# Optimization experiments

Hardware: AMD Instinct MI355X
Metric: run time of the kernel (lower is better)

Reference implementation:

```python
import jax, jax.numpy as jnp
import numpy as np

ALPHA = 0.5
ITER_NUM = 3
SV_NUM = 2
EPS_NORM = 1e-12  # torch F.normalize eps
EPS_DIV = 1e-5
B, D, N = 256, 256, 1024


def _l2norm(t, axis):
    # matches torch F.normalize: t / max(||t||, eps)
    n = jnp.sqrt(jnp.sum(t * t, axis=axis, keepdims=True))
    return t / jnp.maximum(n, EPS_NORM)


def setup_inputs() -> dict:
    key = jax.random.key(0)
    k1, k2 = jax.random.split(key)
    x = jax.random.normal(k1, (B, D, N), dtype=jnp.float32)
    weight = jax.random.normal(k2, (D,), dtype=jnp.float32)
    return {"x": x, "weight": weight}


def reference(x, weight):
    b, d, n = x.shape
    xt = jnp.swapaxes(x, 1, 2)  # (b, N, d) -- matches x.transpose(1, 2)
    us, ss, vs = [], [], []
    s = None
    for _ in range(SV_NUM):  # deflation loop over top singular components
        v = jnp.broadcast_to(weight[None, :, None], (b, d, 1))
        for _ in range(ITER_NUM):  # power iteration
            u = _l2norm(xt @ v, axis=1)                      # (b, N, 1)
            v = _l2norm(jnp.swapaxes(xt, 1, 2) @ u, axis=1)  # (b, d, 1)
        s = jnp.swapaxes(u, 1, 2) @ xt @ v                   # (b, 1, 1) spectral value
        us.append(u)
        ss.append(s.reshape(b, 1))
        vs.append(v)
        # rank-1 deflation: x <- x - u s v^T
        xt = xt - s * (u @ jnp.swapaxes(v, 1, 2))
    U = jnp.concatenate(us, axis=-1)   # (b, N, top)
    V = jnp.concatenate(vs, axis=-1)   # (b, d, top)
    S = jnp.concatenate(ss, axis=-1)   # (b, top)
    # y = U diag(S^alpha) V^T, plus the power-normalized residual
    y = jnp.einsum('bnk,bk,bdk->bnd', U, S ** ALPHA, V)      # (b, N, d)
    y = y + xt / (s ** (1.0 - ALPHA) + EPS_DIV)              # norm_remain branch
    y = jnp.swapaxes(y, 1, 2)                                # (b, d, N)
    return y.reshape(b, -1)                                  # vec == 'full'
```

## Files before the change

### kernel.cpp

```cpp
#include <hip/hip_runtime.h>

#define NB 256
#define ND 256
#define NN 1024

typedef _Float16 f16_t;
typedef _Float16 f16x8 __attribute__((ext_vector_type(8)));
typedef float    f32x4 __attribute__((ext_vector_type(4)));
typedef float    f32x16 __attribute__((ext_vector_type(16)));

__global__ __launch_bounds__(512, 2) void k1_gram(const float* __restrict__ x,
                                                  f16_t* __restrict__ g)
{
    __shared__ __align__(16) f16_t sbuf[2][256 * 64];

    const int t = threadIdx.x;
    const int b = blockIdx.x;
    const float* xb = x + (size_t)b * ND * NN;

    const int c8    = t & 7;
    const int rbase = t >> 3;

    f32x4 pf[8];

    auto issue = [&](int kc) {
        const float* base = xb + (size_t)kc * 64 + c8 * 8;
        #pragma unroll
        for (int kk = 0; kk < 4; ++kk) {
            const float* p = base + (size_t)(rbase + 64 * kk) * NN;
            pf[2 * kk]     = *(const f32x4*)p;
            pf[2 * kk + 1] = *(const f32x4*)(p + 4);
        }
    };
    auto commit = [&](int buf) {
        #pragma unroll
        for (int kk = 0; kk < 4; ++kk) {
            const int row = rbase + 64 * kk;
            f16x8 h;
            #pragma unroll
            for (int j = 0; j < 4; ++j) {
                h[j]     = (f16_t)pf[2 * kk][j];
                h[4 + j] = (f16_t)pf[2 * kk + 1][j];
            }
            *(f16x8*)&sbuf[buf][row * 64 + ((c8 ^ (row & 7)) << 3)] = h;
        }
    };

    const int w     = t >> 6;
    const int lane  = t & 63;
    const int mbase = (w & 3) * 64;
    const int nbase = (w >> 2) * 128;
    const int fr    = lane & 31;
    const int half  = lane >> 5;

    f32x16 acc[2][4] = {};

    issue(0);
    commit(0);

    for (int kc = 0; kc < 16; ++kc) {
        __syncthreads();
        if (kc < 15) issue(kc + 1);
        const f16_t* sb = sbuf[kc & 1];
        #pragma unroll
        for (int ks = 0; ks < 4; ++ks) {
            const int ch = ks * 2 + half;
            f16x8 bf[4];
            #pragma unroll
            for (int nb = 0; nb < 4; ++nb) {
                const int row = nbase + nb * 32 + fr;
                bf[nb] = *(const f16x8*)&sb[row * 64 + ((ch ^ (row & 7)) << 3)];
            }
            #pragma unroll
            for (int mb = 0; mb < 2; ++mb) {
                const int row = mbase + mb * 32 + fr;
                const f16x8 af = *(const f16x8*)&sb[row * 64 + ((ch ^ (row & 7)) << 3)];
                #pragma unroll
                for (int nb = 0; nb < 4; ++nb)
                    acc[mb][nb] = __builtin_amdgcn_mfma_f32_32x32x16_f16(
                        af, bf[nb], acc[mb][nb], 0, 0, 0);
            }
        }
        if (kc < 15) commit((kc + 1) & 1);
    }

    f16_t* gb = g + (size_t)b * ND * ND;
    #pragma unroll
    for (int mb = 0; mb < 2; ++mb)
        #pragma unroll
        for (int nb = 0; nb < 4; ++nb) {
            const int gcol = nbase + nb * 32 + fr;
            #pragma unroll
            for (int r = 0; r < 16; ++r) {
                const int grow = mbase + mb * 32 + (r & 3) + 8 * (r >> 2) + 4 * half;
                gb[grow * ND + gcol] = (f16_t)acc[mb][nb][r];
            }
        }
}

__global__ __launch_bounds__(512, 1) void k2_power(const f16_t* __restrict__ g,
                                                   const float* __restrict__ wvec,
                                                   float* __restrict__ vecs,
                                                   float* __restrict__ pars)
{
    __shared__ float sv[ND];
    __shared__ float sv1[ND];
    __shared__ float sred[8];

    const int t = threadIdx.x;
    const int b = blockIdx.x;
    const int r = t >> 1;
    const int h = t & 1;

    const f16_t* gr = g + (size_t)b * ND * ND + (size_t)r * ND + h * 128;
    f16x8 g8[16];
    #pragma unroll
    for (int i = 0; i < 16; ++i) g8[i] = *(const f16x8*)(gr + i * 8);

    auto reduce = [&](float val) -> float {
        #pragma unroll
        for (int off = 32; off > 0; off >>= 1) val += __shfl_xor(val, off, 64);
        __syncthreads();
        if ((t & 63) == 0) sred[t >> 6] = val;
        __syncthreads();
        float s = 0.f;
        #pragma unroll
        for (int i = 0; i < 8; ++i) s += sred[i];
        return s;
    };

    auto rowdot = [&](void) -> float {
        float acc = 0.f;
        const float* svh = sv + h * 128;
        #pragma unroll
        for (int i = 0; i < 16; ++i) {
            const f32x4 va = *(const f32x4*)&svh[i * 8];
            const f32x4 vb = *(const f32x4*)&svh[i * 8 + 4];
            #pragma unroll
            for (int j = 0; j < 4; ++j) {
                acc += (float)g8[i][j]     * va[j];
                acc += (float)g8[i][4 + j] * vb[j];
            }
        }
        acc += __shfl_xor(acc, 1, 64);
        return acc;
    };

    if (h == 0) sv[r] = wvec[r];
    __syncthreads();

    float s1 = 0.f, n1 = 1.f;
    for (int it = 0; it < 3; ++it) {
        const float p  = rowdot();
        const float pp = reduce(0.5f * p * p);
        const float nrm = fmaxf(sqrtf(pp), 1e-12f);
        if (it == 2) {
            const float pv = reduce(0.5f * p * sv[r]);
            n1 = sqrtf(pv);
            s1 = sqrtf(pp) / n1;
            if (h == 0) {
                vecs[((size_t)b * 4 + 0) * ND + r] = sv[r];
                vecs[((size_t)b * 4 + 2) * ND + r] = p / nrm;
            }
            sv1[r] = p / nrm;
        }
        if (h == 0) sv[r] = p / nrm;
        __syncthreads();
    }

    if (h == 0) sv[r] = wvec[r];
    __syncthreads();

    float s2 = 0.f, n2 = 1.f, d1b = 0.f;
    const float s1sq = s1 * s1;
    for (int it = 0; it < 3; ++it) {
        const float d1 = reduce(0.5f * sv1[r] * sv[r]);
        const float p  = rowdot() - s1sq * d1 * sv1[r];
        const float pp = reduce(0.5f * p * p);
        const float nrm = fmaxf(sqrtf(pp), 1e-12f);
        if (it == 2) {
            const float pv = reduce(0.5f * p * sv[r]);
            n2  = sqrtf(pv);
            s2  = sqrtf(pp) / n2;
            d1b = d1;
            if (h == 0) {
                vecs[((size_t)b * 4 + 1) * ND + r] = sv[r];
                vecs[((size_t)b * 4 + 3) * ND + r] = p / nrm;
            }
        }
        if (h == 0) sv[r] = p / nrm;
        __syncthreads();
    }

    if (t == 0) {
        const float rr = 1.f / (sqrtf(s2) + 1e-5f);
        float* pb = pars + b * 8;
        pb[0] = 1.f / n1;
        pb[1] = 1.f / n2;
        pb[2] = s1 * d1b / n2;
        pb[3] = rr;
        pb[4] = sqrtf(s1) - s1 * rr;
        pb[5] = sqrtf(s2) - s2 * rr;
        pb[6] = s1;
        pb[7] = s2;
    }
}

__global__ __launch_bounds__(256, 2) void k3_out(const float* __restrict__ x,
                                                 const float* __restrict__ vecs,
                                                 const float* __restrict__ pars,
                                                 float* __restrict__ y)
{
    __shared__ float sva[ND], svb[ND], sv1[ND], sv2[ND];
    __shared__ float spr1[16][64], spr2[16][64];
    __shared__ float sg1[64], sg2[64];
    __shared__ float spar[8];

    const int t  = threadIdx.x;
    const int b  = blockIdx.x >> 4;
    const int n0 = (blockIdx.x & 15) * 64;

    {
        const float* vb = vecs + (size_t)b * 4 * ND;
        sva[t] = vb[t];
        svb[t] = vb[ND + t];
        sv1[t] = vb[2 * ND + t];
        sv2[t] = vb[3 * ND + t];
        if (t < 8) spar[t] = pars[b * 8 + t];
    }

    const int c4 = t & 15;
    const int rg = t >> 4;
    const float* xb = x + (size_t)b * ND * NN + n0 + c4 * 4;

    f32x4 xr[16];
    #pragma unroll
    for (int k = 0; k < 16; ++k)
        xr[k] = *(const f32x4*)(xb + (size_t)(rg + 16 * k) * NN);

    __syncthreads();

    f32x4 a1 = {0.f, 0.f, 0.f, 0.f}, a2 = {0.f, 0.f, 0.f, 0.f};
    #pragma unroll
    for (int k = 0; k < 16; ++k) {
        const int row = rg + 16 * k;
        a1 += xr[k] * sva[row];
        a2 += xr[k] * svb[row];
    }
    *(f32x4*)&spr1[rg][c4 * 4] = a1;
    *(f32x4*)&spr2[rg][c4 * 4] = a2;
    __syncthreads();

    if (t < 64) {
        float u1 = 0.f, u2 = 0.f;
        #pragma unroll
        for (int g2 = 0; g2 < 16; ++g2) { u1 += spr1[g2][t]; u2 += spr2[g2][t]; }
        const float uu1 = u1 * spar[0];
        const float uu2 = u2 * spar[1] - spar[2] * uu1;
        sg1[t] = spar[4] * uu1;
        sg2[t] = spar[5] * uu2;
    }
    __syncthreads();

    const float rr = spar[3];
    const f32x4 g1 = *(const f32x4*)&sg1[c4 * 4];
    const f32x4 g2 = *(const f32x4*)&sg2[c4 * 4];
    float* yb = y + (size_t)b * ND * NN + n0 + c4 * 4;
    #pragma unroll
    for (int k = 0; k < 16; ++k) {
        const int row = rg + 16 * k;
        const f32x4 o = xr[k] * rr + g1 * sv1[row] + g2 * sv2[row];
        *(f32x4*)(yb + (size_t)row * NN) = o;
    }
}

extern "C" void kernel_launch(void* const* d_in, const int* in_sizes, int n_in,
                              void* d_out, int out_size, void* d_ws, size_t ws_size,
                              hipStream_t stream)
{
    const float* x = (const float*)d_in[0];
    const float* w = (const float*)d_in[1];
    float* out = (float*)d_out;

    f16_t* G = (f16_t*)d_out;

    float* vecs = (float*)d_ws;
    float* pars = vecs + (size_t)NB * 4 * ND;

    k1_gram<<<dim3(NB), dim3(512), 0, stream>>>(x, G);
    k2_power<<<dim3(NB), dim3(512), 0, stream>>>(G, w, vecs, pars);
    k3_out<<<dim3(NB * 16), dim3(256), 0, stream>>>(x, vecs, pars, out);
}
```

Measured before the change: 545.2 us.

## Fuse Gram, power iteration and output kernels into one per-batch kernel

Merges the three kernels into a single per-batch block. The Gram matrix stays in shared memory with a swizzled layout instead of going through global memory, and the power-iteration vectors and parameters stay in LDS. The output phase loops over 16 column tiles and prefetches the next x tile into registers. This removes the global round trips for G, vecs and pars and two kernel launches. In exchange there are only 256 blocks, LDS use is large (128KB plus extras), which may limit occupancy to one block per CU, and the output phase loses the parallelism of the 4096-block grid.

Result: no change. 549.8 us (+0.9%).

```diff
diff --git a/kernel.cpp b/kernel.cpp
--- a/kernel.cpp
+++ b/kernel.cpp
@@ -9,113 +9,122 @@
 typedef float    f32x4 __attribute__((ext_vector_type(4)));
 typedef float    f32x16 __attribute__((ext_vector_type(16)));
 
-__global__ __launch_bounds__(512, 2) void k1_gram(const float* __restrict__ x,
-                                                  f16_t* __restrict__ g)
+__global__ __launch_bounds__(512, 2) void k_fused(const float* __restrict__ x,
+                                                  const float* __restrict__ wvec,
+                                                  float* __restrict__ y)
 {
-    __shared__ __align__(16) f16_t sbuf[2][256 * 64];
+    __shared__ __align__(16) unsigned char smem[131072];
+    __shared__ float sv[ND], sv1v[ND], sva[ND], svb[ND];
+    __shared__ float sred[8], spar[8], sg1[64], sg2[64];
 
     const int t = threadIdx.x;
     const int b = blockIdx.x;
     const float* xb = x + (size_t)b * ND * NN;
 
-    const int c8    = t & 7;
-    const int rbase = t >> 3;
-
-    f32x4 pf[8];
-
-    auto issue = [&](int kc) {
-        const float* base = xb + (size_t)kc * 64 + c8 * 8;
-        #pragma unroll
-        for (int kk = 0; kk < 4; ++kk) {
-            const float* p = base + (size_t)(rbase + 64 * kk) * NN;
-            pf[2 * kk]     = *(const f32x4*)p;
-            pf[2 * kk + 1] = *(const f32x4*)(p + 4);
-        }
-    };
-    auto commit = [&](int buf) {
-        #pragma unroll
-        for (int kk = 0; kk < 4; ++kk) {
-            const int row = rbase + 64 * kk;
-            f16x8 h;
-            #pragma unroll
-            for (int j = 0; j < 4; ++j) {
-                h[j]     = (f16_t)pf[2 * kk][j];
-                h[4 + j] = (f16_t)pf[2 * kk + 1][j];
-            }
-            *(f16x8*)&sbuf[buf][row * 64 + ((c8 ^ (row & 7)) << 3)] = h;
-        }
-    };
-
-    const int w     = t >> 6;
-    const int lane  = t & 63;
-    const int mbase = (w & 3) * 64;
-    const int nbase = (w >> 2) * 128;
-    const int fr    = lane & 31;
-    const int half  = lane >> 5;
-
-    f32x16 acc[2][4] = {};
-
-    issue(0);
-    commit(0);
-
-    for (int kc = 0; kc < 16; ++kc) {
-        __syncthreads();
-        if (kc < 15) issue(kc + 1);
-        const f16_t* sb = sbuf[kc & 1];
-        #pragma unroll
-        for (int ks = 0; ks < 4; ++ks) {
-            const int ch = ks * 2 + half;
-            f16x8 bf[4];
+    const int w    = t >> 6;
+    const int lane = t & 63;
+    const int fr   = lane & 31;
+    const int half = lane >> 5;
+
+    {
+        f16_t* sb0 = (f16_t*)smem;
+        const int c8    = t & 7;
+        const int rbase = t >> 3;
+        f32x4 pf[8];
+
+        auto issue = [&](int kc) {
+            const float* base = xb + (size_t)kc * 64 + c8 * 8;
+            #pragma unroll
+            for (int kk = 0; kk < 4; ++kk) {
+                const float* p = base + (size_t)(rbase + 64 * kk) * NN;
+                pf[2 * kk]     = *(const f32x4*)p;
+                pf[2 * kk + 1] = *(const f32x4*)(p + 4);
+            }
+        };
+        auto commit = [&](int buf) {
+            #pragma unroll
+            for (int kk = 0; kk < 4; ++kk) {
+                const int row = rbase + 64 * kk;
+                f16x8 hh;
+                #pragma unroll
+                for (int j = 0; j < 4; ++j) {
+                    hh[j]     = (f16_t)pf[2 * kk][j];
+                    hh[4 + j] = (f16_t)pf[2 * kk + 1][j];
+                }
+                *(f16x8*)&sb0[buf * 16384 + row * 64 + ((c8 ^ (row & 7)) << 3)] = hh;
+            }
+        };
+
+        const int mbase = (w & 3) * 64;
+        const int nbase = (w >> 2) * 128;
+
+        f32x16 acc[2][4] = {};
+
+        issue(0);
+        commit(0);
+
+        for (int kc = 0; kc < 16; ++kc) {
+            __syncthreads();
+            if (kc < 15) issue(kc + 1);
+            const f16_t* sb = sb0 + (kc & 1) * 16384;
+            #pragma unroll
+            for (int ks = 0; ks < 4; ++ks) {
+                const int ch = ks * 2 + half;
+                f16x8 bf[4];
+                #pragma unroll
+                for (int nb = 0; nb < 4; ++nb) {
+                    const int row = nbase + nb * 32 + fr;
+                    bf[nb] = *(const f16x8*)&sb[row * 64 + ((ch ^ (row & 7)) << 3)];
+                }
+                #pragma unroll
+                for (int mb = 0; mb < 2; ++mb) {
+                    const int row = mbase + mb * 32 + fr;
+                    const f16x8 af = *(const f16x8*)&sb[row * 64 + ((ch ^ (row & 7)) << 3)];
+                    #pragma unroll
+                    for (int nb = 0; nb < 4; ++nb)
+                        acc[mb][nb] = __builtin_amdgcn_mfma_f32_32x32x16_f16(
+                            af, bf[nb], acc[mb][nb], 0, 0, 0);
+                }
+            }
+            if (kc < 15) commit((kc + 1) & 1);
+        }
+
+        __syncthreads();
+
+        f16_t* G = (f16_t*)smem;
+        #pragma unroll
+        for (int mb = 0; mb < 2; ++mb)
             #pragma unroll
             for (int nb = 0; nb < 4; ++nb) {
-                const int row = nbase + nb * 32 + fr;
-                bf[nb] = *(const f16x8*)&sb[row * 64 + ((ch ^ (row & 7)) << 3)];
-            }
-            #pragma unroll
-            for (int mb = 0; mb < 2; ++mb) {
-                const int row = mbase + mb * 32 + fr;
-                const f16x8 af = *(const f16x8*)&sb[row * 64 + ((ch ^ (row & 7)) << 3)];
-                #pragma unroll
-                for (int nb = 0; nb < 4; ++nb)
-                    acc[mb][nb] = __builtin_amdgcn_mfma_f32_32x32x16_f16(
-                        af, bf[nb], acc[mb][nb], 0, 0, 0);
-            }
-        }
-        if (kc < 15) commit((kc + 1) & 1);
-    }
-
-    f16_t* gb = g + (size_t)b * ND * ND;
-    #pragma unroll
-    for (int mb = 0; mb < 2; ++mb)
-        #pragma unroll
-        for (int nb = 0; nb < 4; ++nb) {
-            const int gcol = nbase + nb * 32 + fr;
-            #pragma unroll
-            for (int r = 0; r < 16; ++r) {
-                const int grow = mbase + mb * 32 + (r & 3) + 8 * (r >> 2) + 4 * half;
-                gb[grow * ND + gcol] = (f16_t)acc[mb][nb][r];
-            }
-        }
-}
-
-__global__ __launch_bounds__(512, 1) void k2_power(const f16_t* __restrict__ g,
-                                                   const float* __restrict__ wvec,
-                                                   float* __restrict__ vecs,
-                                                   float* __restrict__ pars)
-{
-    __shared__ float sv[ND];
-    __shared__ float sv1[ND];
-    __shared__ float sred[8];
-
-    const int t = threadIdx.x;
-    const int b = blockIdx.x;
+                const int gcol = nbase + nb * 32 + fr;
+                const int ci = gcol >> 3, cj = gcol & 7;
+                #pragma unroll
+                for (int reg = 0; reg < 16; ++reg) {
+                    const int grow = mbase + mb * 32 + (reg & 3) + 8 * (reg >> 2) + 4 * half;
+                    G[grow * 256 + ((ci ^ (grow & 7)) << 3) + cj] = (f16_t)acc[mb][nb][reg];
+                }
+            }
+    }
+    __syncthreads();
+
+    const f16_t* G = (const f16_t*)smem;
     const int r = t >> 1;
     const int h = t & 1;
 
-    const f16_t* gr = g + (size_t)b * ND * ND + (size_t)r * ND + h * 128;
     f16x8 g8[16];
     #pragma unroll
-    for (int i = 0; i < 16; ++i) g8[i] = *(const f16x8*)(gr + i * 8);
+    for (int i = 0; i < 16; ++i) {
+        const int c = h * 16 + i;
+        g8[i] = *(const f16x8*)&G[r * 256 + ((c ^ (r & 7)) << 3)];
+    }
+
+    const int c4 = t & 15;
+    const int rg = t >> 4;
+    const float* xb3 = x + (size_t)b * ND * NN + c4 * 4;
+    f32x4 xr[8];
+    #pragma unroll
+    for (int k = 0; k < 8; ++k)
+        xr[k] = *(const f32x4*)(xb3 + (size_t)(rg + 32 * k) * NN);
 
     auto reduce = [&](float val) -> float {
         #pragma unroll
@@ -158,11 +167,8 @@
             const float pv = reduce(0.5f * p * sv[r]);
             n1 = sqrtf(pv);
             s1 = sqrtf(pp) / n1;
-            if (h == 0) {
-                vecs[((size_t)b * 4 + 0) * ND + r] = sv[r];
-                vecs[((size_t)b * 4 + 2) * ND + r] = p / nrm;
-            }
-            sv1[r] = p / nrm;
+            if (h == 0) sva[r] = sv[r];
+            sv1v[r] = p / nrm;
         }
         if (h == 0) sv[r] = p / nrm;
         __syncthreads();
@@ -174,8 +180,8 @@
     float s2 = 0.f, n2 = 1.f, d1b = 0.f;
     const float s1sq = s1 * s1;
     for (int it = 0; it < 3; ++it) {
-        const float d1 = reduce(0.5f * sv1[r] * sv[r]);
-        const float p  = rowdot() - s1sq * d1 * sv1[r];
+        const float d1 = reduce(0.5f * sv1v[r] * sv[r]);
+        const float p  = rowdot() - s1sq * d1 * sv1v[r];
         const float pp = reduce(0.5f * p * p);
         const float nrm = fmaxf(sqrtf(pp), 1e-12f);
         if (it == 2) {
@@ -183,94 +189,78 @@
             n2  = sqrtf(pv);
             s2  = sqrtf(pp) / n2;
             d1b = d1;
-            if (h == 0) {
-                vecs[((size_t)b * 4 + 1) * ND + r] = sv[r];
-                vecs[((size_t)b * 4 + 3) * ND + r] = p / nrm;
-            }
+            if (h == 0) svb[r] = sv[r];
         }
         if (h == 0) sv[r] = p / nrm;
         __syncthreads();
     }
 
     if (t == 0) {
-        const float rr = 1.f / (sqrtf(s2) + 1e-5f);
-        float* pb = pars + b * 8;
-        pb[0] = 1.f / n1;
-        pb[1] = 1.f / n2;
-        pb[2] = s1 * d1b / n2;
-        pb[3] = rr;
-        pb[4] = sqrtf(s1) - s1 * rr;
-        pb[5] = sqrtf(s2) - s2 * rr;
-        pb[6] = s1;
-        pb[7] = s2;
-    }
-}
-
-__global__ __launch_bounds__(256, 2) void k3_out(const float* __restrict__ x,
-                                                 const float* __restrict__ vecs,
-                                                 const float* __restrict__ pars,
-                                                 float* __restrict__ y)
-{
-    __shared__ float sva[ND], svb[ND], sv1[ND], sv2[ND];
-    __shared__ float spr1[16][64], spr2[16][64];
-    __shared__ float sg1[64], sg2[64];
-    __shared__ float spar[8];
-
-    const int t  = threadIdx.x;
-    const int b  = blockIdx.x >> 4;
-    const int n0 = (blockIdx.x & 15) * 64;
-
-    {
-        const float* vb = vecs + (size_t)b * 4 * ND;
-        sva[t] = vb[t];
-        svb[t] = vb[ND + t];
-        sv1[t] = vb[2 * ND + t];
-        sv2[t] = vb[3 * ND + t];
-        if (t < 8) spar[t] = pars[b * 8 + t];
-    }
-
-    const int c4 = t & 15;
-    const int rg = t >> 4;
-    const float* xb = x + (size_t)b * ND * NN + n0 + c4 * 4;
-
-    f32x4 xr[16];
-    #pragma unroll
-    for (int k = 0; k < 16; ++k)
-        xr[k] = *(const f32x4*)(xb + (size_t)(rg + 16 * k) * NN);
-
-    __syncthreads();
-
-    f32x4 a1 = {0.f, 0.f, 0.f, 0.f}, a2 = {0.f, 0.f, 0.f, 0.f};
-    #pragma unroll
-    for (int k = 0; k < 16; ++k) {
-        const int row = rg + 16 * k;
-        a1 += xr[k] * sva[row];
-        a2 += xr[k] * svb[row];
-    }
-    *(f32x4*)&spr1[rg][c4 * 4] = a1;
-    *(f32x4*)&spr2[rg][c4 * 4] = a2;
-    __syncthreads();
-
-    if (t < 64) {
-        float u1 = 0.f, u2 = 0.f;
-        #pragma unroll
-        for (int g2 = 0; g2 < 16; ++g2) { u1 += spr1[g2][t]; u2 += spr2[g2][t]; }
-        const float uu1 = u1 * spar[0];
-        const float uu2 = u2 * spar[1] - spar[2] * uu1;
-        sg1[t] = spar[4] * uu1;
-        sg2[t] = spar[5] * uu2;
-    }
-    __syncthreads();
-
-    const float rr = spar[3];
-    const f32x4 g1 = *(const f32x4*)&sg1[c4 * 4];
-    const f32x4 g2 = *(const f32x4*)&sg2[c4 * 4];
-    float* yb = y + (size_t)b * ND * NN + n0 + c4 * 4;
-    #pragma unroll
-    for (int k = 0; k < 16; ++k) {
-        const int row = rg + 16 * k;
-        const f32x4 o = xr[k] * rr + g1 * sv1[row] + g2 * sv2[row];
-        *(f32x4*)(yb + (size_t)row * NN) = o;
+        const float rrr = 1.f / (sqrtf(s2) + 1e-5f);
+        spar[0] = 1.f / n1;
+        spar[1] = 1.f / n2;
+        spar[2] = s1 * d1b / n2;
+        spar[3] = rrr;
+        spar[4] = sqrtf(s1) - s1 * rrr;
+        spar[5] = sqrtf(s2) - s2 * rrr;
+    }
+    __syncthreads();
+
+    float* spr1 = (float*)smem;
+    float* spr2 = spr1 + 32 * 64;
+
+    const float rr  = spar[3];
+    const float ia1 = spar[0], ia2 = spar[1], k21 = spar[2];
+    const float c1  = spar[4], c2  = spar[5];
+    float* yb = y + (size_t)b * ND * NN + c4 * 4;
+
+    for (int tile = 0; tile < 16; ++tile) {
+        f32x4 a1 = {0.f, 0.f, 0.f, 0.f}, a2 = {0.f, 0.f, 0.f, 0.f};
+        #pragma unroll
+        for (int k = 0; k < 8; ++k) {
+            const int row = rg + 32 * k;
+            a1 += xr[k] * sva[row];
+            a2 += xr[k] * svb[row];
+        }
+        *(f32x4*)&spr1[rg * 64 + c4 * 4] = a1;
+        *(f32x4*)&spr2[rg * 64 + c4 * 4] = a2;
+
+        f32x4 xn[8];
+        if (tile < 15) {
+            const float* xnb = xb3 + (tile + 1) * 64;
+            #pragma unroll
+            for (int k = 0; k < 8; ++k)
+                xn[k] = *(const f32x4*)(xnb + (size_t)(rg + 32 * k) * NN);
+        }
+        __syncthreads();
+
+        if (t < 64) {
+            float u1 = 0.f, u2 = 0.f;
+            #pragma unroll
+            for (int g2 = 0; g2 < 32; ++g2) {
+                u1 += spr1[g2 * 64 + t];
+                u2 += spr2[g2 * 64 + t];
+            }
+            const float uu1 = u1 * ia1;
+            const float uu2 = u2 * ia2 - k21 * uu1;
+            sg1[t] = c1 * uu1;
+            sg2[t] = c2 * uu2;
+        }
+        __syncthreads();
+
+        const f32x4 g1v = *(const f32x4*)&sg1[c4 * 4];
+        const f32x4 g2v = *(const f32x4*)&sg2[c4 * 4];
+        float* yt = yb + tile * 64;
+        #pragma unroll
+        for (int k = 0; k < 8; ++k) {
+            const int row = rg + 32 * k;
+            const f32x4 o = xr[k] * rr + g1v * sv1v[row] + g2v * sv[row];
+            *(f32x4*)(yt + (size_t)row * NN) = o;
+        }
+        if (tile < 15) {
+            #pragma unroll
+            for (int k = 0; k < 8; ++k) xr[k] = xn[k];
+        }
     }
 }
 
@@ -282,12 +272,5 @@
     const float* w = (const float*)d_in[1];
     float* out = (float*)d_out;
 
-    f16_t* G = (f16_t*)d_out;
-
-    float* vecs = (float*)d_ws;
-    float* pars = vecs + (size_t)NB * 4 * ND;
-
-    k1_gram<<<dim3(NB), dim3(512), 0, stream>>>(x, G);
-    k2_power<<<dim3(NB), dim3(512), 0, stream>>>(G, w, vecs, pars);
-    k3_out<<<dim3(NB * 16), dim3(256), 0, stream>>>(x, vecs, pars, out);
+    k_fused<<<dim3(NB), dim3(512), 0, stream>>>(x, w, out);
 }
```
